# Kernel tuning notes

Hardware: AMD Instinct MI355X
Metric: run time of the kernel (lower is better)

Reference implementation:

```python
import jax, jax.numpy as jnp
import numpy as np

N_USERS = 1024
N_ITEMS = 2048
N = N_USERS + N_ITEMS          # 3072 total nodes
D = 128                        # latent_dim_rec
L = 3                          # n_layers
K = [64, 64, 64]               # top-k per layer for getMaskAdj
GAMMA = 0.2                    # residual weight on svd embeddings
X_SCALE = 1.0                  # delta
B = 8192                       # batch of (user, item) pairs


def setup_inputs() -> dict:
    key = jax.random.key(0)
    ks = jax.random.split(key, 9)
    # normalized-adjacency-like dense graph: nonnegative, row sums ~ 1
    A = jax.random.uniform(ks[0], (N, N), dtype=jnp.float32) * (2.0 / N)
    user_emb = jax.random.normal(ks[1], (N_USERS, D), dtype=jnp.float32)
    item_emb = jax.random.normal(ks[2], (N_ITEMS, D), dtype=jnp.float32)
    user_emb0 = jax.random.normal(ks[3], (N_USERS, D), dtype=jnp.float32)
    item_emb0 = jax.random.normal(ks[4], (N_ITEMS, D), dtype=jnp.float32)
    vector_u = jax.random.uniform(ks[5], (1, N), dtype=jnp.float32)
    vector_v = jax.random.uniform(ks[6], (1, N), dtype=jnp.float32)
    users = jax.random.randint(ks[7], (B,), 0, N_USERS)
    items = jax.random.randint(ks[8], (B,), 0, N_ITEMS)
    return {
        "users": users, "items": items, "A": A,
        "user_emb": user_emb, "item_emb": item_emb,
        "user_emb0": user_emb0, "item_emb0": item_emb0,
        "vector_u": vector_u, "vector_v": vector_v,
    }


def topk_mask(M, k):
    """Keep top-k entries per row of M, zero elsewhere (getMaskAdj)."""
    vals, idx = jax.lax.top_k(M, k)          # [N,k], [N,k]
    rows = jnp.arange(M.shape[0])[:, None]
    return jnp.zeros_like(M).at[rows, idx].set(vals)


def _computer(A, user_emb, item_emb, user_emb0, item_emb0, vector_u, vector_v):
    all_emb = jnp.concatenate([user_emb, item_emb], axis=0)      # [N,D]
    all_emb0 = jnp.concatenate([user_emb0, item_emb0], axis=0)   # [N,D]
    u = vector_u[0]  # [N]
    v = vector_v[0]  # [N]

    # ---- computAttention: w_k = u A^k v for k = 0..L (A^0 = I via A_0=eye) ----
    w_list = [jnp.dot(u, v)]
    powers = []           # A^1 .. A^L (g_droped progression)
    Ak = A
    for layer in range(L):
        powers.append(Ak)
        w_list.append(jnp.dot(u, Ak @ v))
        if layer < L - 1:
            Ak = A @ Ak   # g_droped = Graph @ A_k
    w = jnp.stack(w_list)                 # [L+1]
    w = w / jnp.sum(w)
    attention_weight = jax.nn.softmax(w)  # softmax(dim=0)

    # ---- getMaskAdj: top-k masked powers ----
    A_list = [topk_mask(powers[l], K[l]) if K[l] != 0 else powers[l] for l in range(L)]

    # ---- layer-wise propagation with attention-weighted accumulation ----
    emb0 = all_emb
    light_out = X_SCALE * attention_weight[0] * all_emb
    for layer in range(L):
        e = A_list[layer] @ emb0 + GAMMA * all_emb0   # SpMM + residual
        light_out = light_out + X_SCALE * attention_weight[layer + 1] * e
    users_all = light_out[:N_USERS]
    items_all = light_out[N_USERS:]
    return users_all, items_all


def reference(users, items, A, user_emb, item_emb, user_emb0, item_emb0, vector_u, vector_v):
    users_all, items_all = _computer(A, user_emb, item_emb, user_emb0, item_emb0, vector_u, vector_v)
    u_e = users_all[users]   # [B,D]
    i_e = items_all[items]   # [B,D]
    return jnp.sum(u_e * i_e, axis=1)  # [B]
```

## Files before the change

### kernel.cpp

```cpp
#include <hip/hip_runtime.h>
#include <hip/hip_fp8.h>
#include <math.h>

#define NN 3072
#define NU 1024
#define NI 2048
#define DD 128
#define BB 8192
#define GAMMA_F 0.2f

#define SCALE_A 524288.0f
#define F8SCALE2 1.9073486328125e-06f
#define DESCALE38 3.637978807091713e-12f

#define KBLK ((size_t)NN * 64)

typedef __attribute__((ext_vector_type(4))) float f32x4;
typedef __attribute__((ext_vector_type(16))) float f32x16;
typedef __attribute__((ext_vector_type(4))) int i32x4;
typedef __attribute__((ext_vector_type(8))) int i32x8;

static __device__ inline unsigned short bf16bits(float x) {
  union { unsigned u; float f; } cv;
  cv.f = x;
  unsigned r = cv.u + 0x7fff + ((cv.u >> 16) & 1);
  return (unsigned short)(r >> 16);
}

static __device__ inline unsigned pk4_f8(float a, float b, float c, float d) {
#if defined(__has_builtin)
#if __has_builtin(__builtin_amdgcn_cvt_pk_fp8_f32)
  int p = __builtin_amdgcn_cvt_pk_fp8_f32(a, b, 0, false);
  p = __builtin_amdgcn_cvt_pk_fp8_f32(c, d, p, true);
  return (unsigned)p;
#else
  return (unsigned)__hip_fp8_e4m3(a).__x | ((unsigned)__hip_fp8_e4m3(b).__x << 8) |
         ((unsigned)__hip_fp8_e4m3(c).__x << 16) |
         ((unsigned)__hip_fp8_e4m3(d).__x << 24);
#endif
#else
  return (unsigned)__hip_fp8_e4m3(a).__x | ((unsigned)__hip_fp8_e4m3(b).__x << 8) |
         ((unsigned)__hip_fp8_e4m3(c).__x << 16) |
         ((unsigned)__hip_fp8_e4m3(d).__x << 24);
#endif
}

static __device__ inline void atomAddF(float* p, float v) {
#if defined(__has_builtin)
#if __has_builtin(__builtin_amdgcn_global_atomic_fadd_f32)
  __builtin_amdgcn_global_atomic_fadd_f32(
      (__attribute__((address_space(1))) float*)p, v);
#else
  unsafeAtomicAdd(p, v);
#endif
#else
  unsafeAtomicAdd(p, v);
#endif
}

static __device__ inline float block_sum(float s, float* red4) {
  int tid = threadIdx.x;
  for (int off = 32; off; off >>= 1) s += __shfl_down(s, off, 64);
  if ((tid & 63) == 0) red4[tid >> 6] = s;
  __syncthreads();
  return red4[0] + red4[1] + red4[2] + red4[3];
}

static __device__ inline float row_dot_f32(const float* __restrict__ a,
                                           const float* __restrict__ b,
                                           float* red4) {
  const float4* ap = (const float4*)a;
  const float4* bp = (const float4*)b;
  float s = 0.f;
  for (int j = threadIdx.x; j < NN / 4; j += 256) {
    float4 x = ap[j], y = bp[j];
    s += x.x * y.x + x.y * y.y + x.z * y.z + x.w * y.w;
  }
  return block_sum(s, red4);
}

static __device__ inline void load48_bf(const unsigned short* __restrict__ b0,
                                        int parts, int row, int lane,
                                        float* f) {
  const uint4* r0 = (const uint4*)(b0 + (size_t)row * NN);
#pragma unroll
  for (int j = 0; j < 6; ++j) {
    uint4 q = r0[lane + j * 64];
    unsigned uu[4] = {q.x, q.y, q.z, q.w};
#pragma unroll
    for (int e = 0; e < 4; ++e) {
      f[j * 8 + e * 2] = __uint_as_float(uu[e] << 16);
      f[j * 8 + e * 2 + 1] = __uint_as_float(uu[e] & 0xffff0000u);
    }
  }
  for (int p = 1; p < parts; ++p) {
    const uint4* rp = (const uint4*)(b0 + (size_t)p * NN * NN + (size_t)row * NN);
#pragma unroll
    for (int j = 0; j < 6; ++j) {
      uint4 q = rp[lane + j * 64];
      unsigned uu[4] = {q.x, q.y, q.z, q.w};
#pragma unroll
      for (int e = 0; e < 4; ++e) {
        f[j * 8 + e * 2] += __uint_as_float(uu[e] << 16);
        f[j * 8 + e * 2 + 1] += __uint_as_float(uu[e] & 0xffff0000u);
      }
    }
  }
}

static __device__ inline void load48_f32(const float* __restrict__ A, int row,
                                         int lane, float* f) {
  const float4* r0 = (const float4*)(A + (size_t)row * NN);
#pragma unroll
  for (int j = 0; j < 12; ++j) {
    float4 a = r0[lane + j * 64];
    f[j * 4 + 0] = a.x; f[j * 4 + 1] = a.y;
    f[j * 4 + 2] = a.z; f[j * 4 + 3] = a.w;
  }
}

static __device__ void select_compact(const float* f, int lane, float descale,
                                      int bf, int* __restrict__ outCnt,
                                      int* __restrict__ outIdx,
                                      float* __restrict__ outVal) {
  unsigned bor = 0, band = 0xffffffffu;
#pragma unroll
  for (int r = 0; r < 48; ++r) {
    unsigned k = __float_as_uint(f[r]);
    bor |= k; band &= k;
  }
  for (int off = 32; off; off >>= 1) {
    bor |= (unsigned)__shfl_xor((int)bor, off, 64);
    band &= (unsigned)__shfl_xor((int)band, off, 64);
  }
  unsigned diff = bor ^ band;
  int hi = diff ? (31 - __clz(diff)) : 16;
  if (hi < 16) hi = 16;
  if (hi > 30) hi = 30;
  unsigned t = band & ~((2u << hi) - 1u);

  int b = hi;
  while (b >= 17) {
    unsigned base = 1u << (b - 1);
    unsigned cand2 = t | (base << 1);
    int c2 = 0;
#pragma unroll
    for (int r = 0; r < 48; ++r) c2 += (__float_as_uint(f[r]) >= cand2) ? 1 : 0;
    for (int off = 32; off; off >>= 1) c2 += __shfl_xor(c2, off, 64);
    if (c2 >= 64) {
      unsigned cand3 = cand2 | base;
      int c3 = 0;
#pragma unroll
      for (int r = 0; r < 48; ++r)
        c3 += (__float_as_uint(f[r]) >= cand3) ? 1 : 0;
      for (int off = 32; off; off >>= 1) c3 += __shfl_xor(c3, off, 64);
      t = (c3 >= 64) ? cand3 : cand2;
    } else {
      unsigned cand1 = t | base;
      int c1 = 0;
#pragma unroll
      for (int r = 0; r < 48; ++r)
        c1 += (__float_as_uint(f[r]) >= cand1) ? 1 : 0;
      for (int off = 32; off; off >>= 1) c1 += __shfl_xor(c1, off, 64);
      if (c1 >= 64) t = cand1;
    }
    b -= 2;
  }
  if (b == 16) {
    unsigned cand = t | (1u << 16);
    int c = 0;
#pragma unroll
    for (int r = 0; r < 48; ++r) c += (__float_as_uint(f[r]) >= cand) ? 1 : 0;
    for (int off = 32; off; off >>= 1) c += __shfl_xor(c, off, 64);
    if (c >= 64) t = cand;
  }

  int basec = 0;
#pragma unroll
  for (int r = 0; r < 48; ++r) {
    bool keep = __float_as_uint(f[r]) >= t;
    unsigned long long m = __ballot(keep);
    if (keep) {
      int pos = basec + __popcll(m & ((1ull << lane) - 1ull));
      if (pos < 128) {
        int col = bf ? ((r >> 3) * 512 + lane * 8 + (r & 7))
                     : ((r >> 2) * 256 + lane * 4 + (r & 3));
        outIdx[pos] = col << 7;
        outVal[pos] = f[r] * descale;
      }
    }
    basec += __popcll(m);
  }
  if (lane == 0) *outCnt = basec < 128 ? basec : 128;
}

__global__ __launch_bounds__(256) void prep(
    const float* __restrict__ A, const float* __restrict__ vu,
    const float* __restrict__ vv, unsigned char* __restrict__ Af8,
    unsigned char* __restrict__ Atf8, float* __restrict__ y1,
    float* __restrict__ s1, const float* __restrict__ uemb,
    const float* __restrict__ iemb, float* __restrict__ allE) {
  __shared__ float sh[64 * 65 + 512];
  const int bid = blockIdx.x;
  const int t = threadIdx.x;
  if (bid >= 2304) {
    int idx = (bid - 2304) * 256 + t;
    int e = idx * 4;
    float4 v = (e < NU * DD) ? *(const float4*)(uemb + e)
                             : *(const float4*)(iemb + (e - NU * DD));
    *(float4*)(allE + e) = v;
    return;
  }
  const int bx = (bid % 48) * 64, by = (bid / 48) * 64;
  {
    const int r = t >> 2;
    const int ch = t & 3;
    float v16[16];
    const float* arow = A + (size_t)(by + r) * NN + bx + ch * 16;
#pragma unroll
    for (int q4 = 0; q4 < 4; ++q4) {
      float4 val = *(const float4*)(arow + q4 * 4);
      v16[q4 * 4 + 0] = val.x; v16[q4 * 4 + 1] = val.y;
      v16[q4 * 4 + 2] = val.z; v16[q4 * 4 + 3] = val.w;
      float* sp = &sh[r * 65 + ch * 16 + q4 * 4];
      sp[0] = val.x; sp[1] = val.y; sp[2] = val.z; sp[3] = val.w;
    }
    uint4 w;
    w.x = pk4_f8(v16[0] * SCALE_A, v16[1] * SCALE_A, v16[2] * SCALE_A,
                 v16[3] * SCALE_A);
    w.y = pk4_f8(v16[4] * SCALE_A, v16[5] * SCALE_A, v16[6] * SCALE_A,
                 v16[7] * SCALE_A);
    w.z = pk4_f8(v16[8] * SCALE_A, v16[9] * SCALE_A, v16[10] * SCALE_A,
                 v16[11] * SCALE_A);
    w.w = pk4_f8(v16[12] * SCALE_A, v16[13] * SCALE_A, v16[14] * SCALE_A,
                 v16[15] * SCALE_A);
    *(uint4*)(Af8 + (size_t)(bx >> 6) * KBLK + (size_t)(by + r) * 64 +
              ch * 16) = w;
  }
  __syncthreads();
  {
    int c = t >> 2, ch = t & 3;
    float v[16];
#pragma unroll
    for (int e = 0; e < 16; ++e) v[e] = sh[(ch * 16 + e) * 65 + c];
    uint4 w;
    w.x = pk4_f8(v[0] * SCALE_A, v[1] * SCALE_A, v[2] * SCALE_A,
                 v[3] * SCALE_A);
    w.y = pk4_f8(v[4] * SCALE_A, v[5] * SCALE_A, v[6] * SCALE_A,
                 v[7] * SCALE_A);
    w.z = pk4_f8(v[8] * SCALE_A, v[9] * SCALE_A, v[10] * SCALE_A,
                 v[11] * SCALE_A);
    w.w = pk4_f8(v[12] * SCALE_A, v[13] * SCALE_A, v[14] * SCALE_A,
                 v[15] * SCALE_A);
    *(uint4*)(Atf8 + (size_t)(by >> 6) * KBLK + (size_t)(bx + c) * 64 +
              ch * 16) = w;
  }
  const int q = t >> 6;
  const int l = t & 63;
  float sy = 0.f, ss_ = 0.f;
  for (int i = 0; i < 16; ++i) {
    int c = q * 16 + i;
    sy += sh[l * 65 + c] * vv[bx + c];
    ss_ += vu[by + c] * sh[c * 65 + l];
  }
  float* red = sh + 64 * 65;
  red[q * 64 + l] = sy;
  red[256 + q * 64 + l] = ss_;
  __syncthreads();
  if (t < 64) {
    float v4 = red[t] + red[64 + t] + red[128 + t] + red[192 + t];
    atomAddF(&y1[by + t], v4);
  } else if (t < 128) {
    int cc = t - 64;
    float v4 = red[256 + cc] + red[256 + 64 + cc] + red[256 + 128 + cc] +
               red[256 + 192 + cc];
    atomAddF(&s1[bx + cc], v4);
  }
}

static __device__ inline i32x8 ldfragL(const char* p) {
  i32x4 lo = *(const i32x4*)p;
  i32x4 hi = *(const i32x4*)(p + 1024);
  return (i32x8){lo.x, lo.y, lo.z, lo.w, hi.x, hi.y, hi.z, hi.w};
}

__global__ __launch_bounds__(256, 2) void gemm_f8(
    const unsigned char* __restrict__ Ag,
    const unsigned char* __restrict__ Btg,
    unsigned short* __restrict__ Cg) {
  __shared__ char smem[3][24576];
  const int wg = blockIdx.x;
  const int xcd = wg & 7;
  const int idx = wg >> 3;
  const int bxi = xcd * 2 + (idx & 1);
  const int byi = (idx >> 1) & 15;
  const int z = idx >> 5;
  const int rowBase = byi * 192, colBase = bxi * 192;

  const int t = threadIdx.x;
  const int w = t >> 6, l = t & 63;
  const int wr = w >> 1, wc = w & 1;
  const int r32 = l & 31, hh = l >> 5;

  f32x16 acc[3][3];
#pragma unroll
  for (int i = 0; i < 3; ++i)
#pragma unroll
    for (int j = 0; j < 3; ++j)
#pragma unroll
      for (int e = 0; e < 16; ++e) acc[i][j][e] = 0.f;

  const unsigned char* aT = Ag + (size_t)rowBase * 64;
  const unsigned char* bT = Btg + (size_t)colBase * 64;
  const int laneOff = r32 * 64 + hh * 32;
  const int kt0 = z * 24;

#define STAGE(kt, b)                                                        \
  {                                                                         \
    const size_t kOff = (size_t)(kt) * KBLK;                                \
    _Pragma("unroll") for (int r_ = 0; r_ < 6; ++r_) {                      \
      int q_ = r_ * 4 + w;                                                  \
      int qq_ = q_ < 12 ? q_ : q_ - 12;                                     \
      int s_ = qq_ >> 1, h_ = qq_ & 1;                                      \
      const unsigned char* g_ = ((q_ < 12) ? aT : bT) + kOff +              \
                                (size_t)(s_ * 32) * 64 + laneOff + h_ * 16; \
      __builtin_amdgcn_global_load_lds(                                     \
          (const __attribute__((address_space(1))) unsigned*)g_,            \
          (__attribute__((address_space(3))) unsigned*)(smem[b] +           \
                                                        q_ * 1024),         \
          16, 0, 0);                                                        \
    }                                                                       \
  }

  const int ni = 24;
  STAGE(kt0, 0);
  STAGE(kt0 + 1, 1);
  for (int i = 0; i < ni; ++i) {
    if (i < ni - 1) {
      asm volatile("s_waitcnt vmcnt(6)" ::: "memory");
    } else {
      asm volatile("s_waitcnt vmcnt(0)" ::: "memory");
    }
    __builtin_amdgcn_s_barrier();
    __builtin_amdgcn_sched_barrier(0);
    const char* sb = smem[i % 3];
    i32x8 af[3], bfr[3];
#pragma unroll
    for (int ii = 0; ii < 3; ++ii)
      af[ii] = ldfragL(sb + (wr * 3 + ii) * 2048 + l * 16);
#pragma unroll
    for (int j = 0; j < 3; ++j)
      bfr[j] = ldfragL(sb + 12288 + (wc * 3 + j) * 2048 + l * 16);
    if (i + 2 < ni) STAGE(kt0 + i + 2, (i + 2) % 3);
    __builtin_amdgcn_s_setprio(1);
#pragma unroll
    for (int ii = 0; ii < 3; ++ii)
#pragma unroll
      for (int j = 0; j < 3; ++j)
        acc[ii][j] = __builtin_amdgcn_mfma_scale_f32_32x32x64_f8f6f4(
            af[ii], bfr[j], acc[ii][j], 0, 0, 0, 127, 0, 127);
    __builtin_amdgcn_s_setprio(0);
    __builtin_amdgcn_sched_barrier(0);
  }
#undef STAGE

  unsigned short* Cout = Cg + (size_t)z * NN * NN;
#pragma unroll
  for (int i = 0; i < 3; ++i) {
    int rb = rowBase + wr * 96 + i * 32 + 4 * hh;
#pragma unroll
    for (int j = 0; j < 3; ++j) {
      int cc = colBase + wc * 96 + j * 32 + r32;
#pragma unroll
      for (int reg = 0; reg < 16; ++reg) {
        int rr = rb + (reg & 3) + 8 * (reg >> 2);
        Cout[(size_t)rr * NN + cc] = bf16bits(acc[i][j][reg]);
      }
    }
  }
}

__global__ __launch_bounds__(256) void post1(
    const unsigned short* __restrict__ C, int parts,
    const float* __restrict__ A, const float* __restrict__ y1,
    unsigned char* __restrict__ A2f8, int* __restrict__ cnts1,
    int* __restrict__ tIdx1, float* __restrict__ tVal1,
    float* __restrict__ tvec) {
  const int bid = blockIdx.x;
  const int t = threadIdx.x;
  if (bid < 768) {
    int row = bid * 4 + (t >> 6);
    int lane = t & 63;
    float f[48];
    load48_bf(C, parts, row, lane, f);
#pragma unroll
    for (int j = 0; j < 6; ++j) {
      uint2 w;
      w.x = pk4_f8(f[j * 8 + 0] * F8SCALE2, f[j * 8 + 1] * F8SCALE2,
                   f[j * 8 + 2] * F8SCALE2, f[j * 8 + 3] * F8SCALE2);
      w.y = pk4_f8(f[j * 8 + 4] * F8SCALE2, f[j * 8 + 5] * F8SCALE2,
                   f[j * 8 + 6] * F8SCALE2, f[j * 8 + 7] * F8SCALE2);
      size_t addr = (size_t)(j * 8 + (lane >> 3)) * KBLK +
                    (size_t)row * 64 + (lane & 7) * 8;
      *(uint2*)(A2f8 + addr) = w;
    }
    select_compact(f, lane, DESCALE38, 1, &cnts1[row],
                   tIdx1 + (size_t)row * 128, tVal1 + (size_t)row * 128);
  } else {
    int row = (bid - 768) * 4 + (t >> 6);
    int lane = t & 63;
    const float4* rp = (const float4*)(A + (size_t)row * NN);
    const float4* yp = (const float4*)y1;
    float s = 0.f;
#pragma unroll
    for (int j = 0; j < 12; ++j) {
      float4 a = rp[lane + j * 64];
      float4 y = yp[lane + j * 64];
      s += a.x * y.x + a.y * y.y + a.z * y.z + a.w * y.w;
    }
    for (int off = 32; off; off >>= 1) s += __shfl_down(s, off, 64);
    if (lane == 0) tvec[row] = s;
  }
}

__global__ __launch_bounds__(256) void sel02(
    const unsigned short* __restrict__ C, int parts,
    const float* __restrict__ A, int* __restrict__ cnt0,
    int* __restrict__ idx0, float* __restrict__ val0,
    int* __restrict__ cnt2, int* __restrict__ idx2,
    float* __restrict__ val2, const float* __restrict__ vu,
    const float* __restrict__ vv, const float* __restrict__ y1,
    const float* __restrict__ s1, const float* __restrict__ tvec,
    float* __restrict__ wacc) {
  __shared__ float red4[4];
  const int bid = blockIdx.x;
  const int t = threadIdx.x;
  if (bid == 1536) {
    float w0 = row_dot_f32(vu, vv, red4);  __syncthreads();
    float w1 = row_dot_f32(vu, y1, red4);  __syncthreads();
    float w2 = row_dot_f32(s1, y1, red4);  __syncthreads();
    float w3 = row_dot_f32(s1, tvec, red4);
    if (t == 0) { wacc[0] = w0; wacc[1] = w1; wacc[2] = w2; wacc[3] = w3; }
    return;
  }
  const int w = t >> 6, lane = t & 63;
  const int row = (bid >> 1) * 4 + w;
  float f[48];
  if ((bid & 1) == 0) {
    load48_bf(C, parts, row, lane, f);
    select_compact(f, lane, DESCALE38, 1, &cnt2[row],
                   idx2 + (size_t)row * 128, val2 + (size_t)row * 128);
  } else {
    load48_f32(A, row, lane, f);
    select_compact(f, lane, 1.0f, 0, &cnt0[row],
                   idx0 + (size_t)row * 128, val0 + (size_t)row * 128);
  }
}

__global__ __launch_bounds__(256) void gather_light(
    const float* __restrict__ allE, const float* __restrict__ uemb0,
    const float* __restrict__ iemb0, const float* __restrict__ wacc,
    const int* __restrict__ cnt0, const int* __restrict__ idx0,
    const float* __restrict__ val0, const int* __restrict__ cnts1,
    const int* __restrict__ tIdx1, const float* __restrict__ tVal1,
    const int* __restrict__ cnt2, const int* __restrict__ idx2,
    const float* __restrict__ val2, float* __restrict__ lightOut) {
  __shared__ int li[4][384];
  __shared__ float lv[4][384];
  const int t = threadIdx.x;
  const int w = t >> 6, lane = t & 63;
  const int row = blockIdx.x * 4 + w;

  float w0 = wacc[0], w1 = wacc[1], w2 = wacc[2], w3 = wacc[3];
  float ss = w0 + w1 + w2 + w3;
  w0 /= ss; w1 /= ss; w2 /= ss; w3 /= ss;
  float m = fmaxf(fmaxf(w0, w1), fmaxf(w2, w3));
  float ex0 = expf(w0 - m), ex1 = expf(w1 - m), ex2 = expf(w2 - m),
        ex3 = expf(w3 - m);
  float se = ex0 + ex1 + ex2 + ex3;
  float aw0 = ex0 / se, aw1 = ex1 / se, aw2 = ex2 / se, aw3 = ex3 / se;
  float aw4 = GAMMA_F * (aw1 + aw2 + aw3);

  const int c0 = cnt0[row], c1 = cnts1[row], c2 = cnt2[row];
  const int p0 = (c0 + 7) & ~7, p1 = (c1 + 7) & ~7, p2 = (c2 + 7) & ~7;
  int* Li = li[w];
  float* Lv = lv[w];
  const size_t rb = (size_t)row * 128;
  for (int k = lane; k < p0; k += 64) {
    bool in = k < c0;
    Li[k] = in ? idx0[rb + k] : 0;
    Lv[k] = in ? aw1 * val0[rb + k] : 0.f;
  }
  for (int k = lane; k < p1; k += 64) {
    bool in = k < c1;
    Li[p0 + k] = in ? tIdx1[rb + k] : 0;
    Lv[p0 + k] = in ? aw2 * tVal1[rb + k] : 0.f;
  }
  for (int k = lane; k < p2; k += 64) {
    bool in = k < c2;
    Li[p0 + p1 + k] = in ? idx2[rb + k] : 0;
    Lv[p0 + p1 + k] = in ? aw3 * val2[rb + k] : 0.f;
  }

  const int ct = p0 + p1 + p2;
  const float2* E2 = (const float2*)allE;
  float ax = 0.f, ay = 0.f, bx_ = 0.f, by_ = 0.f;
  for (int k = 0; k < ct; k += 8) {
    int i0 = Li[k + 0], i1 = Li[k + 1], i2 = Li[k + 2], i3 = Li[k + 3];
    int i4 = Li[k + 4], i5 = Li[k + 5], i6 = Li[k + 6], i7 = Li[k + 7];
    float v0 = Lv[k + 0], v1 = Lv[k + 1], v2 = Lv[k + 2], v3 = Lv[k + 3];
    float v4 = Lv[k + 4], v5 = Lv[k + 5], v6 = Lv[k + 6], v7 = Lv[k + 7];
    float2 g0 = E2[(i0 >> 1) + lane];
    float2 g1 = E2[(i1 >> 1) + lane];
    float2 g2 = E2[(i2 >> 1) + lane];
    float2 g3 = E2[(i3 >> 1) + lane];
    float2 g4 = E2[(i4 >> 1) + lane];
    float2 g5 = E2[(i5 >> 1) + lane];
    float2 g6 = E2[(i6 >> 1) + lane];
    float2 g7 = E2[(i7 >> 1) + lane];
    ax += v0 * g0.x; ay += v0 * g0.y;
    bx_ += v1 * g1.x; by_ += v1 * g1.y;
    ax += v2 * g2.x; ay += v2 * g2.y;
    bx_ += v3 * g3.x; by_ += v3 * g3.y;
    ax += v4 * g4.x; ay += v4 * g4.y;
    bx_ += v5 * g5.x; by_ += v5 * g5.y;
    ax += v6 * g6.x; ay += v6 * g6.y;
    bx_ += v7 * g7.x; by_ += v7 * g7.y;
  }
  float2 sE = E2[((size_t)row << 6) + lane];
  float2 e0 = (row < NU)
                  ? ((const float2*)uemb0)[(size_t)row * 64 + lane]
                  : ((const float2*)iemb0)[(size_t)(row - NU) * 64 + lane];
  float ox = (ax + bx_) + aw0 * sE.x + aw4 * e0.x;
  float oy = (ay + by_) + aw0 * sE.y + aw4 * e0.y;
  float2 o; o.x = ox; o.y = oy;
  ((float2*)lightOut)[(size_t)row * 64 + lane] = o;
}

__global__ __launch_bounds__(256) void out_dot(const int* __restrict__ users,
                                               const int* __restrict__ items,
                                               const float* __restrict__ lightOut,
                                               float* __restrict__ out) {
  int b = blockIdx.x * 4 + (threadIdx.x >> 6);
  int lane = threadIdx.x & 63;
  const float* up = lightOut + (size_t)users[b] * DD;
  const float* ip = lightOut + (size_t)(NU + items[b]) * DD;
  float s = up[lane] * ip[lane] + up[lane + 64] * ip[lane + 64];
  for (int off = 32; off; off >>= 1) s += __shfl_down(s, off, 64);
  if (lane == 0) out[b] = s;
}

extern "C" void kernel_launch(void* const* d_in, const int* in_sizes, int n_in,
                              void* d_out, int out_size, void* d_ws,
                              size_t ws_size, hipStream_t stream) {
  const int* users = (const int*)d_in[0];
  const int* items = (const int*)d_in[1];
  const float* A = (const float*)d_in[2];
  const float* uemb = (const float*)d_in[3];
  const float* iemb = (const float*)d_in[4];
  const float* uemb0 = (const float*)d_in[5];
  const float* iemb0 = (const float*)d_in[6];
  const float* vu = (const float*)d_in[7];
  const float* vv = (const float*)d_in[8];
  float* out = (float*)d_out;

  char* ws = (char*)d_ws;
  size_t off = 0;
  auto alloc = [&](size_t bytes) -> void* {
    void* p = ws + off;
    off += (bytes + 255) & ~(size_t)255;
    return p;
  };
  unsigned char* Af8 = (unsigned char*)alloc((size_t)NN * NN);
  unsigned char* Atf8 = (unsigned char*)alloc((size_t)NN * NN);
  unsigned char* A2f8 = (unsigned char*)alloc((size_t)NN * NN);
  float* y1 = (float*)alloc((size_t)NN * 4);
  float* s1 = (float*)alloc((size_t)NN * 4);
  float* tvec = (float*)alloc((size_t)NN * 4);
  float* wacc = (float*)alloc(256);
  int* cnts1 = (int*)alloc((size_t)NN * 4);
  int* tIdx1 = (int*)alloc((size_t)NN * 128 * 4);
  float* tVal1 = (float*)alloc((size_t)NN * 128 * 4);
  float* lightOut = (float*)alloc((size_t)NN * DD * 4);
  int* cnt0 = (int*)alloc((size_t)NN * 4);
  int* cnt2 = (int*)alloc((size_t)NN * 4);
  float* allE = (float*)alloc((size_t)NN * DD * 4);

  const size_t LSTB = (size_t)NN * 128 * 4;
  int* idx0 = (int*)(Atf8);
  float* val0 = (float*)(Atf8 + LSTB);
  int* idx2 = (int*)(Atf8 + 2 * LSTB);
  float* val2 = (float*)(Atf8 + 3 * LSTB);

  unsigned short* C = (unsigned short*)alloc((size_t)2 * NN * NN * 2);

  hipMemsetAsync(y1, 0, (size_t)2 * NN * 4, stream);
  prep<<<2688, 256, 0, stream>>>(A, vu, vv, Af8, Atf8, y1, s1, uemb, iemb,
                                 allE);
  gemm_f8<<<512, 256, 0, stream>>>(Af8, Atf8, C);
  post1<<<1536, 256, 0, stream>>>(C, 2, A, y1, A2f8, cnts1, tIdx1, tVal1,
                                  tvec);
  gemm_f8<<<512, 256, 0, stream>>>(A2f8, Atf8, C);
  sel02<<<1537, 256, 0, stream>>>(C, 2, A, cnt0, idx0, val0, cnt2, idx2,
                                  val2, vu, vv, y1, s1, tvec, wacc);
  gather_light<<<768, 256, 0, stream>>>(allE, uemb0, iemb0, wacc, cnt0, idx0,
                                        val0, cnts1, tIdx1, tVal1, cnt2, idx2,
                                        val2, lightOut);
  out_dot<<<BB / 4, 256, 0, stream>>>(users, items, lightOut, out);
}
```

Baseline: 233.6 us.

## Drop split-K in FP8 GEMM and use prefix-scan compaction in top-k select

The FP8 GEMM no longer splits K into two halves written to separate partial buffers. Each of 256 workgroups now runs the full K loop and writes a single bf16 C, so the selection kernels read one buffer instead of summing two partials. This removes half of the C write and read traffic and the bf16 rounding of partial sums, but leaves fewer workgroups than the 256 CUs can hold at two blocks each, so occupancy may drop. Separately, the top-k compaction replaces a per-element ballot/popcount loop with a per-lane count and a wavefront prefix scan.

```diff
diff --git a/kernel.cpp b/kernel.cpp
--- a/kernel.cpp
+++ b/kernel.cpp
@@ -80,8 +80,7 @@
 }
 
 static __device__ inline void load48_bf(const unsigned short* __restrict__ b0,
-                                        int parts, int row, int lane,
-                                        float* f) {
+                                        int row, int lane, float* f) {
   const uint4* r0 = (const uint4*)(b0 + (size_t)row * NN);
 #pragma unroll
   for (int j = 0; j < 6; ++j) {
@@ -91,19 +90,6 @@
     for (int e = 0; e < 4; ++e) {
       f[j * 8 + e * 2] = __uint_as_float(uu[e] << 16);
       f[j * 8 + e * 2 + 1] = __uint_as_float(uu[e] & 0xffff0000u);
-    }
-  }
-  for (int p = 1; p < parts; ++p) {
-    const uint4* rp = (const uint4*)(b0 + (size_t)p * NN * NN + (size_t)row * NN);
-#pragma unroll
-    for (int j = 0; j < 6; ++j) {
-      uint4 q = rp[lane + j * 64];
-      unsigned uu[4] = {q.x, q.y, q.z, q.w};
-#pragma unroll
-      for (int e = 0; e < 4; ++e) {
-        f[j * 8 + e * 2] += __uint_as_float(uu[e] << 16);
-        f[j * 8 + e * 2 + 1] += __uint_as_float(uu[e] & 0xffff0000u);
-      }
     }
   }
 }
@@ -175,23 +161,30 @@
     if (c >= 64) t = cand;
   }
 
-  int basec = 0;
+  int myc = 0;
+#pragma unroll
+  for (int r = 0; r < 48; ++r)
+    myc += (__float_as_uint(f[r]) >= t) ? 1 : 0;
+  int scan = myc;
+  for (int off = 1; off < 64; off <<= 1) {
+    int n = __shfl_up(scan, off, 64);
+    if (lane >= off) scan += n;
+  }
+  int pos = scan - myc;
 #pragma unroll
   for (int r = 0; r < 48; ++r) {
-    bool keep = __float_as_uint(f[r]) >= t;
-    unsigned long long m = __ballot(keep);
-    if (keep) {
-      int pos = basec + __popcll(m & ((1ull << lane) - 1ull));
+    if (__float_as_uint(f[r]) >= t) {
       if (pos < 128) {
         int col = bf ? ((r >> 3) * 512 + lane * 8 + (r & 7))
                      : ((r >> 2) * 256 + lane * 4 + (r & 3));
         outIdx[pos] = col << 7;
         outVal[pos] = f[r] * descale;
       }
-    }
-    basec += __popcll(m);
-  }
-  if (lane == 0) *outCnt = basec < 128 ? basec : 128;
+      ++pos;
+    }
+  }
+  int total = __shfl(scan, 63, 64);
+  if (lane == 0) *outCnt = total < 128 ? total : 128;
 }
 
 __global__ __launch_bounds__(256) void prep(
@@ -284,7 +277,7 @@
   return (i32x8){lo.x, lo.y, lo.z, lo.w, hi.x, hi.y, hi.z, hi.w};
 }
 
-__global__ __launch_bounds__(256, 2) void gemm_f8(
+__global__ __launch_bounds__(256) void gemm_f8(
     const unsigned char* __restrict__ Ag,
     const unsigned char* __restrict__ Btg,
     unsigned short* __restrict__ Cg) {
@@ -293,8 +286,7 @@
   const int xcd = wg & 7;
   const int idx = wg >> 3;
   const int bxi = xcd * 2 + (idx & 1);
-  const int byi = (idx >> 1) & 15;
-  const int z = idx >> 5;
+  const int byi = idx >> 1;
   const int rowBase = byi * 192, colBase = bxi * 192;
 
   const int t = threadIdx.x;
@@ -313,7 +305,6 @@
   const unsigned char* aT = Ag + (size_t)rowBase * 64;
   const unsigned char* bT = Btg + (size_t)colBase * 64;
   const int laneOff = r32 * 64 + hh * 32;
-  const int kt0 = z * 24;
 
 #define STAGE(kt, b)                                                        \
   {                                                                         \
@@ -332,18 +323,18 @@
     }                                                                       \
   }
 
-  const int ni = 24;
-  STAGE(kt0, 0);
-  STAGE(kt0 + 1, 1);
-  for (int i = 0; i < ni; ++i) {
-    if (i < ni - 1) {
+  const int nt = NN / 64;
+  STAGE(0, 0);
+  STAGE(1, 1);
+  for (int kt = 0; kt < nt; ++kt) {
+    if (kt < nt - 1) {
       asm volatile("s_waitcnt vmcnt(6)" ::: "memory");
     } else {
       asm volatile("s_waitcnt vmcnt(0)" ::: "memory");
     }
     __builtin_amdgcn_s_barrier();
     __builtin_amdgcn_sched_barrier(0);
-    const char* sb = smem[i % 3];
+    const char* sb = smem[kt % 3];
     i32x8 af[3], bfr[3];
 #pragma unroll
     for (int ii = 0; ii < 3; ++ii)
@@ -351,7 +342,7 @@
 #pragma unroll
     for (int j = 0; j < 3; ++j)
       bfr[j] = ldfragL(sb + 12288 + (wc * 3 + j) * 2048 + l * 16);
-    if (i + 2 < ni) STAGE(kt0 + i + 2, (i + 2) % 3);
+    if (kt + 2 < nt) STAGE(kt + 2, (kt + 2) % 3);
     __builtin_amdgcn_s_setprio(1);
 #pragma unroll
     for (int ii = 0; ii < 3; ++ii)
@@ -364,7 +355,6 @@
   }
 #undef STAGE
 
-  unsigned short* Cout = Cg + (size_t)z * NN * NN;
 #pragma unroll
   for (int i = 0; i < 3; ++i) {
     int rb = rowBase + wr * 96 + i * 32 + 4 * hh;
@@ -374,25 +364,24 @@
 #pragma unroll
       for (int reg = 0; reg < 16; ++reg) {
         int rr = rb + (reg & 3) + 8 * (reg >> 2);
-        Cout[(size_t)rr * NN + cc] = bf16bits(acc[i][j][reg]);
+        Cg[(size_t)rr * NN + cc] = bf16bits(acc[i][j][reg]);
       }
     }
   }
 }
 
 __global__ __launch_bounds__(256) void post1(
-    const unsigned short* __restrict__ C, int parts,
-    const float* __restrict__ A, const float* __restrict__ y1,
-    unsigned char* __restrict__ A2f8, int* __restrict__ cnts1,
-    int* __restrict__ tIdx1, float* __restrict__ tVal1,
-    float* __restrict__ tvec) {
+    const unsigned short* __restrict__ C, const float* __restrict__ A,
+    const float* __restrict__ y1, unsigned char* __restrict__ A2f8,
+    int* __restrict__ cnts1, int* __restrict__ tIdx1,
+    float* __restrict__ tVal1, float* __restrict__ tvec) {
   const int bid = blockIdx.x;
   const int t = threadIdx.x;
   if (bid < 768) {
     int row = bid * 4 + (t >> 6);
     int lane = t & 63;
     float f[48];
-    load48_bf(C, parts, row, lane, f);
+    load48_bf(C, row, lane, f);
 #pragma unroll
     for (int j = 0; j < 6; ++j) {
       uint2 w;
@@ -424,14 +413,12 @@
 }
 
 __global__ __launch_bounds__(256) void sel02(
-    const unsigned short* __restrict__ C, int parts,
-    const float* __restrict__ A, int* __restrict__ cnt0,
-    int* __restrict__ idx0, float* __restrict__ val0,
-    int* __restrict__ cnt2, int* __restrict__ idx2,
-    float* __restrict__ val2, const float* __restrict__ vu,
-    const float* __restrict__ vv, const float* __restrict__ y1,
-    const float* __restrict__ s1, const float* __restrict__ tvec,
-    float* __restrict__ wacc) {
+    const unsigned short* __restrict__ C, const float* __restrict__ A,
+    int* __restrict__ cnt0, int* __restrict__ idx0, float* __restrict__ val0,
+    int* __restrict__ cnt2, int* __restrict__ idx2, float* __restrict__ val2,
+    const float* __restrict__ vu, const float* __restrict__ vv,
+    const float* __restrict__ y1, const float* __restrict__ s1,
+    const float* __restrict__ tvec, float* __restrict__ wacc) {
   __shared__ float red4[4];
   const int bid = blockIdx.x;
   const int t = threadIdx.x;
@@ -447,7 +434,7 @@
   const int row = (bid >> 1) * 4 + w;
   float f[48];
   if ((bid & 1) == 0) {
-    load48_bf(C, parts, row, lane, f);
+    load48_bf(C, row, lane, f);
     select_compact(f, lane, DESCALE38, 1, &cnt2[row],
                    idx2 + (size_t)row * 128, val2 + (size_t)row * 128);
   } else {
@@ -592,17 +579,16 @@
   int* idx2 = (int*)(Atf8 + 2 * LSTB);
   float* val2 = (float*)(Atf8 + 3 * LSTB);
 
-  unsigned short* C = (unsigned short*)alloc((size_t)2 * NN * NN * 2);
+  unsigned short* C = (unsigned short*)alloc((size_t)NN * NN * 2);
 
   hipMemsetAsync(y1, 0, (size_t)2 * NN * 4, stream);
   prep<<<2688, 256, 0, stream>>>(A, vu, vv, Af8, Atf8, y1, s1, uemb, iemb,
                                  allE);
-  gemm_f8<<<512, 256, 0, stream>>>(Af8, Atf8, C);
-  post1<<<1536, 256, 0, stream>>>(C, 2, A, y1, A2f8, cnts1, tIdx1, tVal1,
-                                  tvec);
-  gemm_f8<<<512, 256, 0, stream>>>(A2f8, Atf8, C);
-  sel02<<<1537, 256, 0, stream>>>(C, 2, A, cnt0, idx0, val0, cnt2, idx2,
-                                  val2, vu, vv, y1, s1, tvec, wacc);
+  gemm_f8<<<256, 256, 0, stream>>>(Af8, Atf8, C);
+  post1<<<1536, 256, 0, stream>>>(C, A, y1, A2f8, cnts1, tIdx1, tVal1, tvec);
+  gemm_f8<<<256, 256, 0, stream>>>(A2f8, Atf8, C);
+  sel02<<<1537, 256, 0, stream>>>(C, A, cnt0, idx0, val0, cnt2, idx2, val2,
+                                  vu, vv, y1, s1, tvec, wacc);
   gather_light<<<768, 256, 0, stream>>>(allE, uemb0, iemb0, wacc, cnt0, idx0,
                                         val0, cnts1, tIdx1, tVal1, cnt2, idx2,
                                         val2, lightOut);
```

Result: no change. 231.9 us (-0.7%).
